# Kernel optimization log

Measured on AMD Instinct MI355X. Metric: run time of the kernel, lower is better.

Reference implementation:

```python
import jax, jax.numpy as jnp
import numpy as np

N_WIN = 8  # matches init kwarg n_win

def setup_inputs() -> dict:
    key = jax.random.key(0)
    k1, k2, k3 = jax.random.split(key, 3)
    c = 64
    x = jax.random.normal(k1, (1, c, 256, 256), dtype=jnp.float32)
    W = jax.random.normal(k2, (3 * c, c), dtype=jnp.float32) * 0.05
    bias = jax.random.normal(k3, (3 * c,), dtype=jnp.float32) * 0.05
    return {"x": x, "W": W, "bias": bias}

def reference(x, W, bias):
    b, c, h, w = x.shape
    n_h = n_w = N_WIN
    hs, ws = h // n_h, w // n_w
    nw = n_h * n_w
    # unfold into non-overlapping windows: [1, nw, hs*ws, c]
    xw = x.reshape(b, c, n_h, hs, n_w, ws)
    xw = xw.transpose(0, 2, 4, 3, 5, 1).reshape(1, nw, hs * ws, c)
    # shared QKV linear
    qkv = xw @ W.T + bias
    q, k, v = qkv[..., :c], qkv[..., c:2 * c], qkv[..., 2 * c:3 * c]
    # region-level routing via mean-pooled tokens
    q_r = q.mean(axis=2)  # [1, nw, c]
    k_r = k.mean(axis=2)
    a_r = jax.nn.relu(jnp.einsum('bic,bjc->bij', q_r, k_r))  # [1, nw, nw]
    # mix windows: a_r @ flattened(k/q) == window-mixing einsum
    k_m = jnp.einsum('bij,bjtc->bitc', a_r, k)
    q_m = jnp.einsum('bij,bjtc->bitc', a_r, q)
    # relu-gated windowed attention
    attn = jax.nn.relu(jnp.einsum('bitc,bisc->bits', q_m, k_m))  # [1, nw, T, T]
    o = jnp.einsum('bits,bisc->bitc', attn, v)  # [1, nw, T, c]
    # fold back to image
    o = o.reshape(b, n_h, n_w, hs, ws, c).transpose(0, 5, 1, 3, 2, 4).reshape(b, c, h, w)
    return o
```

## Files before the change

### kernel.cpp

```cpp
#include <hip/hip_runtime.h>

typedef _Float16 half_t;
typedef __attribute__((ext_vector_type(8))) _Float16 half8;
typedef __attribute__((ext_vector_type(4))) _Float16 half4;
typedef __attribute__((ext_vector_type(4))) float floatx4;
typedef __attribute__((ext_vector_type(16))) float floatx16;

#define MFMA16(A, B, C) __builtin_amdgcn_mfma_f32_16x16x32_f16((A), (B), (C), 0, 0, 0)
#define MFMA32(A, B, C) __builtin_amdgcn_mfma_f32_32x32x16_f16((A), (B), (C), 0, 0, 0)

__global__ __launch_bounds__(256) void k_qkv(
    const float* __restrict__ x, const float* __restrict__ W,
    const float* __restrict__ bias, half_t* __restrict__ q,
    half_t* __restrict__ k, half_t* __restrict__ vT,
    float* __restrict__ qsum, float* __restrict__ ksum) {
  __shared__ __align__(16) char smem[52736];
  half_t(*Xs)[72] = (half_t(*)[72])smem;
  half_t(*Ws)[72] = (half_t(*)[72])(smem + 18432);
  half_t(*S1)[136] = (half_t(*)[136])smem;
  half_t(*S2)[136] = (half_t(*)[136])(smem + 34816);
  float* qs_l = (float*)(smem + 52224);
  float* ks_l = qs_l + 64;
  const int w = blockIdx.y;
  const int tx = blockIdx.x;
  const int t0 = tx * 128;
  const int ih = w >> 3, iw = w & 7;
  const int xbase = ih * 8192 + iw * 32 + tx * 1024;
  const int tid = threadIdx.x;

  for (int i = tid; i < 2048; i += 256) {
    const int c = i >> 5, g = i & 31;
    const int tt = (g >> 3) * 32 + (g & 7) * 4;
    const floatx4 v =
        *(const floatx4*)&x[c * 65536 + xbase + (g >> 3) * 256 + (g & 7) * 4];
    #pragma unroll
    for (int p = 0; p < 4; p++) Xs[tt + p][c] = (half_t)v[p];
  }
  for (int i = tid; i < 3072; i += 256) {
    const int o = i >> 4, c4 = (i & 15) * 4;
    const floatx4 v = *(const floatx4*)&W[o * 64 + c4];
    half4 hv;
    #pragma unroll
    for (int p = 0; p < 4; p++) hv[p] = (half_t)v[p];
    *(half4*)&Ws[o][c4] = hv;
  }
  if (tid < 64) { qs_l[tid] = 0.f; ks_l[tid] = 0.f; }
  __syncthreads();

  const int wave = tid >> 6, lane = tid & 63;
  const int lrow = lane & 15, lq = lane >> 4;
  const int rbase = (wave >> 1) * 64;
  const int cbase = (wave & 1) * 96;

  floatx4 acc[4][6];
  const floatx4 z = {0.f, 0.f, 0.f, 0.f};
  #pragma unroll
  for (int mt = 0; mt < 4; mt++)
    #pragma unroll
    for (int nt = 0; nt < 6; nt++) acc[mt][nt] = z;

  #pragma unroll
  for (int kf = 0; kf < 2; kf++) {
    const int koff = kf * 32 + lq * 8;
    half8 a[4], b[6];
    #pragma unroll
    for (int mt = 0; mt < 4; mt++)
      a[mt] = *(const half8*)&Xs[rbase + mt * 16 + lrow][koff];
    #pragma unroll
    for (int nt = 0; nt < 6; nt++)
      b[nt] = *(const half8*)&Ws[cbase + nt * 16 + lrow][koff];
    #pragma unroll
    for (int mt = 0; mt < 4; mt++)
      #pragma unroll
      for (int nt = 0; nt < 6; nt++)
        acc[mt][nt] = MFMA16(a[mt], b[nt], acc[mt][nt]);
  }
  __syncthreads();

  #pragma unroll
  for (int nt = 0; nt < 6; nt++) {
    const int o = cbase + nt * 16 + lrow;
    const float bs = bias[o];
    if (o < 128) {
      float s = 0.f;
      #pragma unroll
      for (int mt = 0; mt < 4; mt++) {
        const int tr = rbase + mt * 16 + lq * 4;
        #pragma unroll
        for (int r = 0; r < 4; r++) {
          const float v = acc[mt][nt][r] + bs;
          S1[tr + r][o] = (half_t)v;
          s += v;
        }
      }
      if (o < 64) atomicAdd(&qs_l[o], s);
      else atomicAdd(&ks_l[o - 64], s);
    } else {
      const int oc = o - 128;
      #pragma unroll
      for (int mt = 0; mt < 4; mt++) {
        const int tr = rbase + mt * 16 + lq * 4;
        half4 pk;
        #pragma unroll
        for (int r = 0; r < 4; r++) pk[r] = (half_t)(acc[mt][nt][r] + bs);
        *(half4*)&S2[oc][tr] = pk;
      }
    }
  }
  __syncthreads();

  for (int idx = tid; idx < 3072; idx += 256) {
    if (idx < 2048) {
      const int t = idx >> 4, seg = idx & 15;
      const half8 v = *(const half8*)&S1[t][seg * 8];
      if (seg < 8)
        *(half8*)&q[w * 65536 + (t0 + t) * 64 + seg * 8] = v;
      else
        *(half8*)&k[w * 65536 + (t0 + t) * 64 + (seg - 8) * 8] = v;
    } else {
      const int i2 = idx - 2048;
      const int oc = i2 >> 4, seg = i2 & 15;
      *(half8*)&vT[w * 65536 + oc * 1024 + t0 + seg * 8] =
          *(const half8*)&S2[oc][seg * 8];
    }
  }
  if (tid < 64) {
    atomicAdd(&qsum[w * 64 + tid], qs_l[tid]);
    atomicAdd(&ksum[w * 64 + tid], ks_l[tid]);
  }
}

__global__ __launch_bounds__(256) void k_mix(const half_t* __restrict__ q,
                                             const half_t* __restrict__ k,
                                             const float* __restrict__ qsum,
                                             const float* __restrict__ ksum,
                                             half_t* __restrict__ qm,
                                             half_t* __restrict__ km) {
  __shared__ __align__(16) half_t qh[64][72];
  __shared__ __align__(16) half_t kh[64][72];
  __shared__ __align__(16) half_t arL[64][72];
  const half_t* __restrict__ src = blockIdx.y ? k : q;
  half_t* __restrict__ dst = blockIdx.y ? km : qm;
  const int tid = threadIdx.x;
  const int wave = tid >> 6, lane = tid & 63;
  const int ln31 = lane & 31;
  const int hk8 = (lane >> 5) * 8;
  const int lrow = lane & 15, lq = lane >> 4;

  const int pos0 = blockIdx.x * 256 + wave * 64 + ln31;
  half8 bB0[4];
  #pragma unroll
  for (int kk = 0; kk < 4; kk++)
    #pragma unroll
    for (int jj = 0; jj < 8; jj++)
      bB0[kk][jj] = src[(kk * 16 + hk8 + jj) * 65536 + pos0];

  for (int e = tid; e < 1024; e += 256) {
    const int i = e >> 4, c4 = (e & 15) * 4;
    const floatx4 sq = *(const floatx4*)&qsum[i * 64 + c4];
    const floatx4 sk = *(const floatx4*)&ksum[i * 64 + c4];
    #pragma unroll
    for (int p = 0; p < 4; p++) {
      qh[i][c4 + p] = (half_t)sq[p];
      kh[i][c4 + p] = (half_t)sk[p];
    }
  }
  __syncthreads();

  {
    floatx4 ac[4];
    const floatx4 z = {0.f, 0.f, 0.f, 0.f};
    #pragma unroll
    for (int nt = 0; nt < 4; nt++) ac[nt] = z;
    #pragma unroll
    for (int kf = 0; kf < 2; kf++) {
      const int koff = kf * 32 + lq * 8;
      const half8 aF = *(const half8*)&qh[wave * 16 + lrow][koff];
      #pragma unroll
      for (int nt = 0; nt < 4; nt++) {
        const half8 bF = *(const half8*)&kh[nt * 16 + lrow][koff];
        ac[nt] = MFMA16(aF, bF, ac[nt]);
      }
    }
    const float scale = 1.f / (1024.f * 1024.f);
    #pragma unroll
    for (int nt = 0; nt < 4; nt++)
      #pragma unroll
      for (int r = 0; r < 4; r++) {
        const float v = ac[nt][r] * scale;
        arL[wave * 16 + lq * 4 + r][nt * 16 + lrow] =
            (half_t)(v > 0.f ? v : 0.f);
      }
  }
  __syncthreads();

  half8 aA[2][4];
  #pragma unroll
  for (int mt = 0; mt < 2; mt++)
    #pragma unroll
    for (int kk = 0; kk < 4; kk++)
      aA[mt][kk] = *(const half8*)&arL[mt * 32 + ln31][kk * 16 + hk8];

  #pragma unroll
  for (int t32 = 0; t32 < 2; t32++) {
    const int pos = blockIdx.x * 256 + wave * 64 + t32 * 32 + ln31;
    half8 bB[4];
    if (t32 == 0) {
      #pragma unroll
      for (int kk = 0; kk < 4; kk++) bB[kk] = bB0[kk];
    } else {
      #pragma unroll
      for (int kk = 0; kk < 4; kk++)
        #pragma unroll
        for (int jj = 0; jj < 8; jj++)
          bB[kk][jj] = src[(kk * 16 + hk8 + jj) * 65536 + pos];
    }

    floatx16 c0, c1;
    #pragma unroll
    for (int r = 0; r < 16; r++) { c0[r] = 0.f; c1[r] = 0.f; }
    #pragma unroll
    for (int kk = 0; kk < 4; kk++) {
      c0 = MFMA32(aA[0][kk], bB[kk], c0);
      c1 = MFMA32(aA[1][kk], bB[kk], c1);
    }
    const int h4 = (lane >> 5) * 4;
    #pragma unroll
    for (int r = 0; r < 16; r++) {
      const int row = (r & 3) + h4 + 8 * (r >> 2);
      dst[row * 65536 + pos] = (half_t)c0[r];
      dst[(32 + row) * 65536 + pos] = (half_t)c1[r];
    }
  }
}

__global__ __launch_bounds__(256, 2) void k_attn(const half_t* __restrict__ qm,
                                                 const half_t* __restrict__ km,
                                                 const half_t* __restrict__ vT,
                                                 float* __restrict__ out) {
  __shared__ __align__(16) half_t Vs[64][136];
  __shared__ __align__(16) half_t St[128][138];
  const int w = blockIdx.x;
  const int t0 = blockIdx.y * 128;
  const int tid = threadIdx.x;
  const int wave = tid >> 6, lane = tid & 63;
  const int ln31 = lane & 31;
  const int hk8 = (lane >> 5) * 8, hk4 = (lane >> 5) * 4;
  const int w32 = wave * 32;
  const int wbase = w * 65536;

  half8 bQ[4][4];
  #pragma unroll
  for (int tt = 0; tt < 4; tt++)
    #pragma unroll
    for (int kk = 0; kk < 4; kk++)
      bQ[tt][kk] = *(const half8*)&qm[wbase + (t0 + tt * 32 + ln31) * 64 +
                                      kk * 16 + hk8];

  floatx16 oacc[2];
  #pragma unroll
  for (int ct = 0; ct < 2; ct++)
    #pragma unroll
    for (int r = 0; r < 16; r++) oacc[ct][r] = 0.f;

  half8 vpre[4], aK[4];
  #pragma unroll
  for (int j = 0; j < 4; j++) {
    const int idx = j * 256 + tid;
    const int c = idx >> 4, so = (idx & 15) * 8;
    vpre[j] = *(const half8*)&vT[wbase + c * 1024 + so];
  }
  #pragma unroll
  for (int kk = 0; kk < 4; kk++)
    aK[kk] = *(const half8*)&km[wbase + (w32 + ln31) * 64 + kk * 16 + hk8];

  for (int sc = 0; sc < 8; sc++) {
    floatx16 sacc[4];
    #pragma unroll
    for (int tt = 0; tt < 4; tt++)
      #pragma unroll
      for (int r = 0; r < 16; r++) sacc[tt][r] = 0.f;
    __builtin_amdgcn_s_setprio(1);
    #pragma unroll
    for (int kk = 0; kk < 4; kk++)
      #pragma unroll
      for (int tt = 0; tt < 4; tt++)
        sacc[tt] = MFMA32(aK[kk], bQ[tt][kk], sacc[tt]);
    __builtin_amdgcn_s_setprio(0);

    __syncthreads();

    #pragma unroll
    for (int j = 0; j < 4; j++) {
      const int idx = j * 256 + tid;
      const int c = idx >> 4, so = (idx & 15) * 8;
      *(half8*)&Vs[c][so] = vpre[j];
    }
    #pragma unroll
    for (int tt = 0; tt < 4; tt++) {
      const int t = tt * 32 + ln31;
      #pragma unroll
      for (int g = 0; g < 4; g++) {
        const int s = w32 + g * 8 + hk4;
        half4 pk;
        #pragma unroll
        for (int p = 0; p < 4; p++) {
          const float v = sacc[tt][g * 4 + p];
          pk[p] = (half_t)(v > 0.f ? v : 0.f);
        }
        *(half4*)&St[t][s] = pk;
      }
    }
    half8 aKn[4];
    if (sc < 7) {
      const int s0n = (sc + 1) * 128;
      #pragma unroll
      for (int j = 0; j < 4; j++) {
        const int idx = j * 256 + tid;
        const int c = idx >> 4, so = (idx & 15) * 8;
        vpre[j] = *(const half8*)&vT[wbase + c * 1024 + s0n + so];
      }
      #pragma unroll
      for (int kk = 0; kk < 4; kk++)
        aKn[kk] = *(const half8*)&km[wbase + (s0n + w32 + ln31) * 64 +
                                     kk * 16 + hk8];
    }
    __syncthreads();

    __builtin_amdgcn_s_setprio(1);
    #pragma unroll
    for (int kk = 0; kk < 8; kk++) {
      const half8 bS = *(const half8*)&St[w32 + ln31][kk * 16 + hk8];
      #pragma unroll
      for (int ct = 0; ct < 2; ct++) {
        const half8 aV = *(const half8*)&Vs[ct * 32 + ln31][kk * 16 + hk8];
        oacc[ct] = MFMA32(aV, bS, oacc[ct]);
      }
    }
    __builtin_amdgcn_s_setprio(0);
    if (sc < 7) {
      #pragma unroll
      for (int kk = 0; kk < 4; kk++) aK[kk] = aKn[kk];
    }
  }

  const int ih = w >> 3, iw = w & 7;
  const int obase = ih * 8192 + iw * 32;
  const int tb = ((t0 + w32) >> 5) * 256 + ln31;
  const int h4 = (lane >> 5) * 4;
  #pragma unroll
  for (int ct = 0; ct < 2; ct++) {
    #pragma unroll
    for (int r = 0; r < 16; r++) {
      const int c = ct * 32 + (r & 3) + h4 + 8 * (r >> 2);
      out[c * 65536 + obase + tb] = oacc[ct][r];
    }
  }
}

extern "C" void kernel_launch(void* const* d_in, const int* in_sizes, int n_in,
                              void* d_out, int out_size, void* d_ws, size_t ws_size,
                              hipStream_t stream) {
  const float* x = (const float*)d_in[0];
  const float* W = (const float*)d_in[1];
  const float* bias = (const float*)d_in[2];
  float* out = (float*)d_out;

  half_t* q = (half_t*)d_ws;
  half_t* k = q + 4194304;
  half_t* vT = k + 4194304;
  half_t* qm = vT + 4194304;
  half_t* km = qm + 4194304;
  float* qsum = (float*)(km + 4194304);
  float* ksum = qsum + 4096;

  hipMemsetAsync(qsum, 0, 2 * 4096 * sizeof(float), stream);
  k_qkv<<<dim3(8, 64), 256, 0, stream>>>(x, W, bias, q, k, vT, qsum, ksum);
  k_mix<<<dim3(256, 2), 256, 0, stream>>>(q, k, qsum, ksum, qm, km);
  k_attn<<<dim3(64, 8), 256, 0, stream>>>(qm, km, vT, out);
}
```

Baseline: 115.8 us.

## XOR-swizzle attention LDS tiles and hoist mix-kernel global loads

The attention kernel's Vs and St shared-memory tiles switch from padded 2D arrays to a byte buffer addressed with an XOR swizzle on 16-byte chunks, keyed on the row index. This is meant to cut LDS bank conflicts on the half4 score stores and the half8 MFMA operand reads. In the mix kernel, the global loads for both 32-column sub-tiles are now issued up front, before the routing computation, so their latency is hidden. That costs more registers per thread. The St row stride goes from 276 to 288 bytes, so shared memory per block grows slightly.

```diff
diff --git a/kernel.cpp b/kernel.cpp
--- a/kernel.cpp
+++ b/kernel.cpp
@@ -148,12 +148,15 @@
   const int lrow = lane & 15, lq = lane >> 4;
 
   const int pos0 = blockIdx.x * 256 + wave * 64 + ln31;
-  half8 bB0[4];
-  #pragma unroll
-  for (int kk = 0; kk < 4; kk++)
-    #pragma unroll
-    for (int jj = 0; jj < 8; jj++)
-      bB0[kk][jj] = src[(kk * 16 + hk8 + jj) * 65536 + pos0];
+  half8 bB[2][4];
+  #pragma unroll
+  for (int t32 = 0; t32 < 2; t32++)
+    #pragma unroll
+    for (int kk = 0; kk < 4; kk++)
+      #pragma unroll
+      for (int jj = 0; jj < 8; jj++)
+        bB[t32][kk][jj] =
+            src[(kk * 16 + hk8 + jj) * 65536 + pos0 + t32 * 32];
 
   for (int e = tid; e < 1024; e += 256) {
     const int i = e >> 4, c4 = (e & 15) * 4;
@@ -203,26 +206,14 @@
 
   #pragma unroll
   for (int t32 = 0; t32 < 2; t32++) {
-    const int pos = blockIdx.x * 256 + wave * 64 + t32 * 32 + ln31;
-    half8 bB[4];
-    if (t32 == 0) {
-      #pragma unroll
-      for (int kk = 0; kk < 4; kk++) bB[kk] = bB0[kk];
-    } else {
-      #pragma unroll
-      for (int kk = 0; kk < 4; kk++)
-        #pragma unroll
-        for (int jj = 0; jj < 8; jj++)
-          bB[kk][jj] = src[(kk * 16 + hk8 + jj) * 65536 + pos];
-    }
-
+    const int pos = pos0 + t32 * 32;
     floatx16 c0, c1;
     #pragma unroll
     for (int r = 0; r < 16; r++) { c0[r] = 0.f; c1[r] = 0.f; }
     #pragma unroll
     for (int kk = 0; kk < 4; kk++) {
-      c0 = MFMA32(aA[0][kk], bB[kk], c0);
-      c1 = MFMA32(aA[1][kk], bB[kk], c1);
+      c0 = MFMA32(aA[0][kk], bB[t32][kk], c0);
+      c1 = MFMA32(aA[1][kk], bB[t32][kk], c1);
     }
     const int h4 = (lane >> 5) * 4;
     #pragma unroll
@@ -238,8 +229,9 @@
                                                  const half_t* __restrict__ km,
                                                  const half_t* __restrict__ vT,
                                                  float* __restrict__ out) {
-  __shared__ __align__(16) half_t Vs[64][136];
-  __shared__ __align__(16) half_t St[128][138];
+  __shared__ __align__(16) char smem[55296];
+  char* const VsB = smem;
+  char* const StB = smem + 18432;
   const int w = blockIdx.x;
   const int t0 = blockIdx.y * 128;
   const int tid = threadIdx.x;
@@ -249,6 +241,13 @@
   const int w32 = wave * 32;
   const int wbase = w * 65536;
 
+  auto vs_ptr = [&](int c, int sbyte) -> char* {
+    return VsB + c * 288 + (sbyte ^ ((c & 15) << 4));
+  };
+  auto st_ptr = [&](int t, int sbyte) -> char* {
+    return StB + t * 288 + (sbyte ^ ((t & 15) << 4));
+  };
+
   half8 bQ[4][4];
   #pragma unroll
   for (int tt = 0; tt < 4; tt++)
@@ -293,8 +292,8 @@
     #pragma unroll
     for (int j = 0; j < 4; j++) {
       const int idx = j * 256 + tid;
-      const int c = idx >> 4, so = (idx & 15) * 8;
-      *(half8*)&Vs[c][so] = vpre[j];
+      const int c = idx >> 4;
+      *(half8*)vs_ptr(c, (idx & 15) * 16) = vpre[j];
     }
     #pragma unroll
     for (int tt = 0; tt < 4; tt++) {
@@ -308,7 +307,7 @@
           const float v = sacc[tt][g * 4 + p];
           pk[p] = (half_t)(v > 0.f ? v : 0.f);
         }
-        *(half4*)&St[t][s] = pk;
+        *(half4*)st_ptr(t, s * 2) = pk;
       }
     }
     half8 aKn[4];
@@ -330,10 +329,11 @@
     __builtin_amdgcn_s_setprio(1);
     #pragma unroll
     for (int kk = 0; kk < 8; kk++) {
-      const half8 bS = *(const half8*)&St[w32 + ln31][kk * 16 + hk8];
+      const half8 bS = *(const half8*)st_ptr(w32 + ln31, (kk * 16 + hk8) * 2);
       #pragma unroll
       for (int ct = 0; ct < 2; ct++) {
-        const half8 aV = *(const half8*)&Vs[ct * 32 + ln31][kk * 16 + hk8];
+        const half8 aV =
+            *(const half8*)vs_ptr(ct * 32 + ln31, (kk * 16 + hk8) * 2);
         oacc[ct] = MFMA32(aV, bS, oacc[ct]);
       }
     }
```

Result: no change. 116.4 us (+0.5%).
